# Kernel optimization log

Hardware: AMD Instinct MI355X
Metric: run time of the kernel (lower is better)

## Reference

```python
import jax, jax.numpy as jnp
import numpy as np

D_MODEL = 1024
N_HIDDEN = 64   # per-head dim (outer factor of packed proj dim)
N_HEAD = 16
B, L = 2, 2048


def setup_inputs() -> dict:
    key = jax.random.key(0)
    ks = jax.random.split(key, 7)
    s = 0.02
    return {
        "q": jax.random.normal(ks[0], (B, L, D_MODEL), dtype=jnp.float32),
        "k": jax.random.normal(ks[1], (B, L, D_MODEL), dtype=jnp.float32),
        "v": jax.random.normal(ks[2], (B, L, D_MODEL), dtype=jnp.float32),
        # torch nn.Linear weights: shape (out_features, in_features), y = x @ W.T
        "W_Q": jax.random.normal(ks[3], (N_HIDDEN * N_HEAD, D_MODEL), dtype=jnp.float32) * s,
        "W_K": jax.random.normal(ks[4], (N_HIDDEN * N_HEAD, D_MODEL), dtype=jnp.float32) * s,
        "W_V": jax.random.normal(ks[5], (N_HIDDEN * N_HEAD, D_MODEL), dtype=jnp.float32) * s,
        "W_O": jax.random.normal(ks[6], (D_MODEL, N_HEAD * N_HIDDEN), dtype=jnp.float32) * s,
    }


def reference(q, k, v, W_Q, W_K, W_V, W_O):
    b, l, _ = q.shape
    # projections (bias=False)
    qp = q @ W_Q.T  # [b,l,n_hidden*n_head]
    kp = k @ W_K.T
    vp = v @ W_V.T
    # rearrange 'b l (c h) -> b l c h' with c=n_hidden: hidden is OUTER factor
    qh = qp.reshape(b, l, N_HIDDEN, N_HEAD)
    kh = kp.reshape(b, l, N_HIDDEN, N_HEAD)
    vh = vp.reshape(b, l, N_HIDDEN, N_HEAD)
    scores = jnp.einsum('bldh,bjdh->bhlj', qh, kh) / np.float32(np.sqrt(N_HIDDEN))
    attn = jax.nn.softmax(scores, axis=-1)
    out = jnp.einsum('bhlj,bjdh->bldh', attn, vh)  # [b,l,n_hidden,n_head]
    out = out.reshape(b, l, N_HIDDEN * N_HEAD)      # 'b l d h -> b l (d h)'
    return out @ W_O.T
```

## Files before the change

### kernel.cpp

```cpp
#include <hip/hip_runtime.h>
#include <hip/hip_bf16.h>
#include <stdint.h>

typedef __attribute__((ext_vector_type(8))) short short8;
typedef __attribute__((ext_vector_type(4))) float f32x4;
typedef __attribute__((ext_vector_type(16))) float f32x16;
typedef __attribute__((ext_vector_type(2))) int int2v;
typedef unsigned short u16;
typedef unsigned int u32;


#define WAIT_VM12() do { asm volatile("s_waitcnt vmcnt(12)" ::: "memory"); \
                         __builtin_amdgcn_sched_barrier(0); } while (0)
#define WAIT_VM8()  do { asm volatile("s_waitcnt vmcnt(8)" ::: "memory"); \
                         __builtin_amdgcn_sched_barrier(0); } while (0)
#define WAIT_VM0()  do { asm volatile("s_waitcnt vmcnt(0)" ::: "memory"); \
                         __builtin_amdgcn_sched_barrier(0); } while (0)
#define BARRIER()   do { __builtin_amdgcn_s_barrier(); \
                         __builtin_amdgcn_sched_barrier(0); } while (0)
#define LGKM0_BAR() do { asm volatile("s_waitcnt lgkmcnt(0)" ::: "memory"); \
                         __builtin_amdgcn_s_barrier(); \
                         __builtin_amdgcn_sched_barrier(0); } while (0)

#define FSWZ(r) (((r) ^ ((r) >> 3)) & 7)

__device__ __forceinline__ u16 bf16rne(float f) {
  u32 u = __builtin_bit_cast(u32, f);
  u += 0x7FFFu + ((u >> 16) & 1u);
  return (u16)(u >> 16);
}

__device__ __forceinline__ u32 cvtpk(float lo, float hi) {
  u32 r;
  asm("v_cvt_pk_bf16_f32 %0, %1, %2" : "=v"(r) : "v"(lo), "v"(hi));
  return r;
}

__device__ __forceinline__ void gl_lds16(const u16* g, u16* l) {
  __builtin_amdgcn_global_load_lds((const __attribute__((address_space(1))) void*)g,
                                   (__attribute__((address_space(3))) void*)l, 16, 0, 0);
}

struct CastArgs {
  const float* src[4];
  u16* dst[4];
  int n4[4];
};

__global__ void cast_all(CastArgs a) {
  const int id = blockIdx.y;
  const float* __restrict__ s = a.src[id];
  u16* __restrict__ d = a.dst[id];
  const int stride = gridDim.x * blockDim.x;
  const int i0 = blockIdx.x * blockDim.x + threadIdx.x;
  if (id < 3) {
    const int n4 = a.n4[id];
    for (int i = i0; i < n4; i += stride) {
      float4 v = ((const float4*)s)[i];
      u32 lo = (u32)bf16rne(v.x) | ((u32)bf16rne(v.y) << 16);
      u32 hi = (u32)bf16rne(v.z) | ((u32)bf16rne(v.w) << 16);
      ((uint2*)d)[i] = make_uint2(lo, hi);
    }
  } else {
    const int n = a.n4[3];
    for (int i = i0; i < n; i += stride) {
      int row = i >> 10, c = i & 1023;
      int hh = c >> 6, dd = c & 63;
      d[i] = bf16rne(s[(row << 10) + dd * 16 + hh]);
    }
  }
}

struct ProjFArgs { const float* A[3]; const u16* W[3]; u16* D[3]; float scale[3]; };

__global__ __launch_bounds__(256, 2) void gemm_projf(ProjFArgs pa) {
  const int bid = blockIdx.x;
  const int grp = ((bid >> 6) << 3) | (bid & 7);
  const int bn = ((bid >> 3) & 7) * 128;
  const int z = grp >> 5;
  const int bm = (grp & 31) * 128;
  const float* __restrict__ A = pa.A[z];
  const u16* __restrict__ Bw = pa.W[z];
  u16* __restrict__ D = pa.D[z];
  const float ascale = pa.scale[z];
  const int epi = (z == 2) ? 1 : 0;

  const int tid = threadIdx.x, lane = tid & 63, w = tid >> 6;
  const int wr = w >> 1, wc = w & 1;
  __shared__ __align__(16) u16 As[2][128 * 64];
  __shared__ __align__(16) u16 Bs[2][128 * 64];

  f32x4 acc[4][4];
#pragma unroll
  for (int m = 0; m < 4; ++m)
#pragma unroll
    for (int n = 0; n < 4; ++n) acc[m][n] = (f32x4){0.f, 0.f, 0.f, 0.f};

  struct ARegs { float4 v[8]; };
  ARegs RA, RB;

  auto STAGE_A = [&](int kt, ARegs& R) {
#pragma unroll
    for (int i = 0; i < 4; ++i) {
      int c = tid + i * 256;
      int row = c >> 3;
      int col = (((c & 7) ^ (row & 7)) << 3);
      const float* src = A + (size_t)(bm + row) * 1024 + kt * 64 + col;
      R.v[2 * i] = *(const float4*)(src);
      R.v[2 * i + 1] = *(const float4*)(src + 4);
    }
  };
  auto WRITE_A = [&](ARegs& R, int b) {
#pragma unroll
    for (int i = 0; i < 4; ++i) {
      int c = tid + i * 256;
      u32 p0 = (u32)bf16rne(R.v[2 * i].x) | ((u32)bf16rne(R.v[2 * i].y) << 16);
      u32 p1 = (u32)bf16rne(R.v[2 * i].z) | ((u32)bf16rne(R.v[2 * i].w) << 16);
      u32 p2 = (u32)bf16rne(R.v[2 * i + 1].x) | ((u32)bf16rne(R.v[2 * i + 1].y) << 16);
      u32 p3 = (u32)bf16rne(R.v[2 * i + 1].z) | ((u32)bf16rne(R.v[2 * i + 1].w) << 16);
      *(uint4*)&As[b][c * 8] = make_uint4(p0, p1, p2, p3);
    }
  };
  auto STAGE_B = [&](int kt, int b) {
#pragma unroll
    for (int i = 0; i < 4; ++i) {
      int c = tid + i * 256;
      int row = c >> 3;
      int swz = (((c & 7) ^ (row & 7)) << 3);
      gl_lds16(Bw + (size_t)(bn + row) * 1024 + kt * 64 + swz, &Bs[b][c * 8]);
    }
  };
  auto COMPUTE = [&](int b) {
#pragma unroll
    for (int ks = 0; ks < 2; ++ks) {
      const int ck = ks * 4 + (lane >> 4);
      short8 af[4], bfr[4];
#pragma unroll
      for (int m = 0; m < 4; ++m) {
        int r = wr * 64 + m * 16 + (lane & 15);
        af[m] = *(const short8*)&As[b][(r * 8 + (ck ^ (r & 7))) * 8];
      }
#pragma unroll
      for (int n = 0; n < 4; ++n) {
        int r = wc * 64 + n * 16 + (lane & 15);
        bfr[n] = *(const short8*)&Bs[b][(r * 8 + (ck ^ (r & 7))) * 8];
      }
#pragma unroll
      for (int m = 0; m < 4; ++m)
#pragma unroll
        for (int n = 0; n < 4; ++n)
          acc[m][n] = __builtin_amdgcn_mfma_f32_16x16x32_bf16(af[m], bfr[n], acc[m][n], 0, 0, 0);
    }
  };

  STAGE_A(0, RA); STAGE_B(0, 0);
  STAGE_A(1, RB); STAGE_B(1, 1);
  for (int k2 = 0; k2 < 7; ++k2) {
    const int kt = 2 * k2;
    WAIT_VM12();
    WRITE_A(RA, 0); LGKM0_BAR();
    COMPUTE(0); BARRIER();
    STAGE_A(kt + 2, RA); STAGE_B(kt + 2, 0);
    WAIT_VM12();
    WRITE_A(RB, 1); LGKM0_BAR();
    COMPUTE(1); BARRIER();
    STAGE_A(kt + 3, RB); STAGE_B(kt + 3, 1);
  }
  WAIT_VM12();
  WRITE_A(RA, 0); LGKM0_BAR();
  COMPUTE(0); BARRIER();
  WAIT_VM0();
  WRITE_A(RB, 1); LGKM0_BAR();
  COMPUTE(1);

  const int lrow4 = (lane >> 4) << 2;
  const int h = lane & 15;
  if (epi == 0) {
    const int dbase = (bn + wc * 64) >> 4;
#pragma unroll
    for (int m = 0; m < 4; ++m)
#pragma unroll
      for (int i = 0; i < 4; ++i) {
        int R = bm + wr * 64 + m * 16 + lrow4 + i;
        int b = R >> 11, l = R & 2047;
        u32 lo = (u32)bf16rne(acc[m][0][i] * ascale) | ((u32)bf16rne(acc[m][1][i] * ascale) << 16);
        u32 hi = (u32)bf16rne(acc[m][2][i] * ascale) | ((u32)bf16rne(acc[m][3][i] * ascale) << 16);
        size_t addr = ((size_t)((b * 16 + h) * 2048 + l)) * 64 + dbase;
        *(uint2*)(D + addr) = make_uint2(lo, hi);
      }
  } else {
    const int dbase = (bn + wc * 64) >> 4;
    const int b = bm >> 11;
#pragma unroll
    for (int m = 0; m < 4; ++m) {
      int l0 = (bm & 2047) + wr * 64 + m * 16 + lrow4;
#pragma unroll
      for (int n = 0; n < 4; ++n) {
        int d = dbase + n;
        u32 lo = (u32)bf16rne(acc[m][n][0]) | ((u32)bf16rne(acc[m][n][1]) << 16);
        u32 hi = (u32)bf16rne(acc[m][n][2]) | ((u32)bf16rne(acc[m][n][3]) << 16);
        size_t addr = ((size_t)((b * 16 + h) * 64 + d)) * 2048 + l0;
        *(uint2*)(D + addr) = make_uint2(lo, hi);
      }
    }
  }
}

__global__ __launch_bounds__(256, 2) void gemm_oproj(const u16* __restrict__ A,
                                                     const u16* __restrict__ Bw,
                                                     float* __restrict__ C) {
  const int bid = blockIdx.x;
  const int slot = bid >> 3;
  const int bm = ((bid & 7) * 4 + (slot >> 3)) * 128;
  const int bn = (slot & 7) * 128;
  const int tid = threadIdx.x, lane = tid & 63, w = tid >> 6;
  const int wr = w >> 1, wc = w & 1;
  __shared__ __align__(16) u16 As[2][128 * 64];
  __shared__ __align__(16) u16 Bs[2][128 * 64];
  f32x4 acc[4][4];
#pragma unroll
  for (int m = 0; m < 4; ++m)
#pragma unroll
    for (int n = 0; n < 4; ++n) acc[m][n] = (f32x4){0.f, 0.f, 0.f, 0.f};

  auto STAGE = [&](int kt, int b) {
#pragma unroll
    for (int i = 0; i < 4; ++i) {
      int c = tid + i * 256;
      int row = c >> 3, kc = c & 7;
      int swz = (kc ^ (row & 7)) << 3;
      int bA = bm >> 11;
      int lrow = (bm & 2047) + row;
      const u16* srcA = A + ((size_t)(bA * 16 + kt) * 2048 + lrow) * 64 + swz;
      gl_lds16(srcA, &As[b][c * 8]);
      const u16* srcB = Bw + (size_t)(bn + row) * 1024 + kt * 64 + swz;
      gl_lds16(srcB, &Bs[b][c * 8]);
    }
  };

  auto COMPUTE = [&](int b) {
#pragma unroll
    for (int ks = 0; ks < 2; ++ks) {
      const int ck = ks * 4 + (lane >> 4);
      short8 af[4], bfr[4];
#pragma unroll
      for (int m = 0; m < 4; ++m) {
        int r = wr * 64 + m * 16 + (lane & 15);
        af[m] = *(const short8*)&As[b][(r * 8 + (ck ^ (r & 7))) * 8];
      }
#pragma unroll
      for (int n = 0; n < 4; ++n) {
        int r = wc * 64 + n * 16 + (lane & 15);
        bfr[n] = *(const short8*)&Bs[b][(r * 8 + (ck ^ (r & 7))) * 8];
      }
#pragma unroll
      for (int m = 0; m < 4; ++m)
#pragma unroll
        for (int n = 0; n < 4; ++n)
          acc[m][n] = __builtin_amdgcn_mfma_f32_16x16x32_bf16(af[m], bfr[n], acc[m][n], 0, 0, 0);
    }
  };

  STAGE(0, 0);
  STAGE(1, 1);
  for (int kt = 0; kt < 15; ++kt) {
    WAIT_VM8();
    BARRIER();
    COMPUTE(kt & 1);
    BARRIER();
    if (kt < 14) STAGE(kt + 2, kt & 1);
  }
  WAIT_VM0();
  BARRIER();
  COMPUTE(1);

  const int lrow4 = (lane >> 4) << 2;
#pragma unroll
  for (int m = 0; m < 4; ++m)
#pragma unroll
    for (int i = 0; i < 4; ++i) {
      int R = bm + wr * 64 + m * 16 + lrow4 + i;
      size_t base = (size_t)R * 1024 + bn + wc * 64 + (lane & 15);
#pragma unroll
      for (int n = 0; n < 4; ++n) C[base + n * 16] = acc[m][n][i];
    }
}

__global__ __launch_bounds__(128, 2) void attn_kernel(const u16* __restrict__ Qh,
                                                      const u16* __restrict__ Kh,
                                                      const u16* __restrict__ Vt,
                                                      u16* __restrict__ Oh) {
  const int hb = blockIdx.x;
  const int qt = blockIdx.y;
  const int tid = threadIdx.x, lane = tid & 63, w = tid >> 6;
  const int l31 = lane & 31, hi = lane >> 5;
  __shared__ __align__(16) u16 Ks[2][64 * 64];
  __shared__ __align__(16) u16 Vs[3][64 * 64];

  const u16* Qg = Qh + (size_t)hb * (2048 * 64);
  const u16* Kg = Kh + (size_t)hb * (2048 * 64);
  const u16* Vg = Vt + (size_t)hb * (64 * 2048);
  const int qrow = qt * 64 + w * 32 + l31;

  short8 qf[4];
#pragma unroll
  for (int ks = 0; ks < 4; ++ks)
    qf[ks] = *(const short8*)(Qg + (size_t)qrow * 64 + ks * 16 + hi * 8);

  int rs[4], sw[4];
#pragma unroll
  for (int i = 0; i < 4; ++i) {
    int c = tid + i * 128;
    rs[i] = c >> 3;
    sw[i] = (((c & 7) ^ FSWZ(rs[i])) << 3);
  }

  auto STAGE_K = [&](int t, int slot) {
    const size_t ko = (size_t)t * (64 * 64);
#pragma unroll
    for (int i = 0; i < 4; ++i) {
      int c = tid + i * 128;
      gl_lds16(Kg + ko + (size_t)rs[i] * 64 + sw[i], &Ks[slot][c * 8]);
    }
  };
  auto STAGE_V = [&](int t, int slot) {
    const int vo = t * 64;
#pragma unroll
    for (int i = 0; i < 4; ++i) {
      int c = tid + i * 128;
      gl_lds16(Vg + (size_t)rs[i] * 2048 + vo + sw[i], &Vs[slot][c * 8]);
    }
  };

  f32x16 oacc0, oacc1, SA0, SA1, SB0, SB1;
#pragma unroll
  for (int i = 0; i < 16; ++i) { oacc0[i] = 0.f; oacc1[i] = 0.f; }
  u32 pkA[16], pkB[16];
  float lrow = 0.f;

  auto QKT = [&](int kslot, f32x16& s0, f32x16& s1) {
#pragma unroll
    for (int i = 0; i < 16; ++i) { s0[i] = 0.f; s1[i] = 0.f; }
    __builtin_amdgcn_s_setprio(1);
#pragma unroll
    for (int ks = 0; ks < 4; ++ks) {
      const int ck = 2 * ks + hi;
      const int r0 = l31, r1 = 32 + l31;
      short8 k0 = *(const short8*)&Ks[kslot][(r0 * 8 + (ck ^ FSWZ(r0))) * 8];
      short8 k1 = *(const short8*)&Ks[kslot][(r1 * 8 + (ck ^ FSWZ(r1))) * 8];
      s0 = __builtin_amdgcn_mfma_f32_32x32x16_bf16(k0, qf[ks], s0, 0, 0, 0);
      s1 = __builtin_amdgcn_mfma_f32_32x32x16_bf16(k1, qf[ks], s1, 0, 0, 0);
    }
    __builtin_amdgcn_s_setprio(0);
  };

  auto PV = [&](const u32* pk, int vslot) {
    __builtin_amdgcn_s_setprio(1);
#pragma unroll
    for (int c = 0; c < 4; ++c) {
      union { u32 wu[4]; short8 v; } un;
      un.wu[0] = pk[c * 4 + 0]; un.wu[1] = pk[c * 4 + 1];
      un.wu[2] = pk[c * 4 + 2]; un.wu[3] = pk[c * 4 + 3];
      const int ckv = 2 * c + hi;
      const int rv0 = l31, rv1 = 32 + l31;
      short8 v0 = *(const short8*)&Vs[vslot][(rv0 * 8 + (ckv ^ FSWZ(rv0))) * 8];
      short8 v1 = *(const short8*)&Vs[vslot][(rv1 * 8 + (ckv ^ FSWZ(rv1))) * 8];
      oacc0 = __builtin_amdgcn_mfma_f32_32x32x16_bf16(v0, un.v, oacc0, 0, 0, 0);
      oacc1 = __builtin_amdgcn_mfma_f32_32x32x16_bf16(v1, un.v, oacc1, 0, 0, 0);
    }
    __builtin_amdgcn_s_setprio(0);
  };

  auto SOFTMAX = [&](f32x16& s0, f32x16& s1, u32* pk) {
#pragma unroll
    for (int i = 0; i < 16; ++i) {
      s0[i] = __builtin_amdgcn_exp2f(s0[i]);
      s1[i] = __builtin_amdgcn_exp2f(s1[i]);
    }
    f32x16 a01 = s0 + s1;
    float r8[8];
#pragma unroll
    for (int i = 0; i < 8; ++i) r8[i] = a01[i] + a01[i + 8];
#pragma unroll
    for (int i = 0; i < 4; ++i) r8[i] += r8[i + 4];
    float rsum = (r8[0] + r8[1]) + (r8[2] + r8[3]);
    int2v pr = __builtin_amdgcn_permlane32_swap(__builtin_bit_cast(int, rsum),
                                                __builtin_bit_cast(int, rsum), false, false);
    lrow += __builtin_bit_cast(float, pr[0]) + __builtin_bit_cast(float, pr[1]);
#pragma unroll
    for (int c = 0; c < 4; ++c) {
      float pe0, pe1, pe2, pe3, pe4, pe5, pe6, pe7;
      if (c < 2) {
        const int s8 = (c & 1) * 8;
        pe0 = s0[s8 + 0]; pe1 = s0[s8 + 1]; pe2 = s0[s8 + 2]; pe3 = s0[s8 + 3];
        pe4 = s0[s8 + 4]; pe5 = s0[s8 + 5]; pe6 = s0[s8 + 6]; pe7 = s0[s8 + 7];
      } else {
        const int s8 = (c & 1) * 8;
        pe0 = s1[s8 + 0]; pe1 = s1[s8 + 1]; pe2 = s1[s8 + 2]; pe3 = s1[s8 + 3];
        pe4 = s1[s8 + 4]; pe5 = s1[s8 + 5]; pe6 = s1[s8 + 6]; pe7 = s1[s8 + 7];
      }
      u32 a0 = cvtpk(pe0, pe1), a1 = cvtpk(pe2, pe3);
      u32 a2 = cvtpk(pe4, pe5), a3 = cvtpk(pe6, pe7);
      int2v w02 = __builtin_amdgcn_permlane32_swap((int)a0, (int)a2, false, false);
      int2v w13 = __builtin_amdgcn_permlane32_swap((int)a1, (int)a3, false, false);
      pk[c * 4 + 0] = (u32)w02[0]; pk[c * 4 + 1] = (u32)w13[0];
      pk[c * 4 + 2] = (u32)w02[1]; pk[c * 4 + 3] = (u32)w13[1];
    }
  };

  STAGE_K(0, 0); STAGE_K(1, 1); STAGE_V(0, 0);
  WAIT_VM8(); BARRIER();
  QKT(0, SA0, SA1);
  BARRIER();
  STAGE_K(2, 0); STAGE_V(1, 1);
  WAIT_VM8(); BARRIER();
  QKT(1, SB0, SB1);
  SOFTMAX(SA0, SA1, pkB);
  BARRIER();
  STAGE_K(3, 1); STAGE_V(2, 2);

  for (int i = 2; i < 32; i += 2) {
    WAIT_VM8(); BARRIER();
    QKT(0, SA0, SA1);
    PV(pkB, (i - 2) % 3);
    SOFTMAX(SB0, SB1, pkA);
    BARRIER();
    if (i + 2 <= 31) STAGE_K(i + 2, 0);
    STAGE_V(i + 1, (i + 1) % 3);
    WAIT_VM8(); BARRIER();
    QKT(1, SB0, SB1);
    PV(pkA, (i - 1) % 3);
    SOFTMAX(SA0, SA1, pkB);
    BARRIER();
    if (i + 3 <= 31) STAGE_K(i + 3, 1);
    if (i + 2 <= 31) STAGE_V(i + 2, (i + 2) % 3);
  }

  WAIT_VM0(); BARRIER();
  SOFTMAX(SB0, SB1, pkA);
  PV(pkB, 30 % 3);
  PV(pkA, 31 % 3);

  const float inv = 1.0f / lrow;
  u16* Og = Oh + (size_t)hb * (2048 * 64) + (size_t)qrow * 64;
#pragma unroll
  for (int dblk = 0; dblk < 2; ++dblk) {
#pragma unroll
    for (int r = 0; r < 16; r += 2) {
      const int d = dblk * 32 + (r & 3) + 8 * (r >> 2) + 4 * hi;
      float v0 = (dblk ? oacc1[r] : oacc0[r]) * inv;
      float v1 = (dblk ? oacc1[r + 1] : oacc0[r + 1]) * inv;
      *(u32*)(Og + d) = (u32)bf16rne(v0) | ((u32)bf16rne(v1) << 16);
    }
  }
}

extern "C" void kernel_launch(void* const* d_in, const int* in_sizes, int n_in,
                              void* d_out, int out_size, void* d_ws, size_t ws_size,
                              hipStream_t stream) {
  const float* q = (const float*)d_in[0];
  const float* k = (const float*)d_in[1];
  const float* v = (const float*)d_in[2];
  const float* WQ = (const float*)d_in[3];
  const float* WK = (const float*)d_in[4];
  const float* WV = (const float*)d_in[5];
  const float* WO = (const float*)d_in[6];
  float* out = (float*)d_out;
  char* ws = (char*)d_ws;
  const size_t MB = 1024 * 1024;
  if (ws_size < 64 * MB) return;

  u16* WQb = (u16*)(ws + 24 * MB);
  u16* WKb = (u16*)(ws + 26 * MB);
  u16* WVb = (u16*)(ws + 28 * MB);
  u16* WOt = (u16*)(ws + 30 * MB);
  u16* Qh  = (u16*)(ws + 32 * MB);
  u16* Kh  = (u16*)(ws + 40 * MB);
  u16* Vt  = (u16*)(ws + 48 * MB);
  u16* Ohd = (u16*)(ws + 56 * MB);

  CastArgs ca;
  ca.src[0] = WQ; ca.dst[0] = WQb; ca.n4[0] = (1024 * 1024) / 4;
  ca.src[1] = WK; ca.dst[1] = WKb; ca.n4[1] = (1024 * 1024) / 4;
  ca.src[2] = WV; ca.dst[2] = WVb; ca.n4[2] = (1024 * 1024) / 4;
  ca.src[3] = WO; ca.dst[3] = WOt; ca.n4[3] = 1024 * 1024;
  cast_all<<<dim3(128, 4), 256, 0, stream>>>(ca);

  ProjFArgs pa;
  pa.A[0] = q; pa.W[0] = WQb; pa.D[0] = Qh;  pa.scale[0] = 0.18033688011f;
  pa.A[1] = k; pa.W[1] = WKb; pa.D[1] = Kh;  pa.scale[1] = 1.0f;
  pa.A[2] = v; pa.W[2] = WVb; pa.D[2] = Vt;  pa.scale[2] = 1.0f;
  gemm_projf<<<768, 256, 0, stream>>>(pa);

  attn_kernel<<<dim3(32, 32), 128, 0, stream>>>(Qh, Kh, Vt, Ohd);

  gemm_oproj<<<256, 256, 0, stream>>>(Ohd, WOt, out);
}
```

Baseline: 128.5 us.

## Reorder GEMM main loop to overlap LDS writes and loads with MFMA compute

Restructures the double-buffered projection GEMM loop so each iteration waits once, issues the next B stage and A prefetch, writes the other A buffer to LDS, and then computes on the current buffer. This drops the separate barrier after each compute and lets LDS writes and global loads proceed alongside the MFMA work. In exchange it waits for all outstanding loads (vmcnt(0)) each half-iteration instead of vmcnt(12), which can expose global load latency, and the buffer hazards now depend on a single barrier per step.

```diff
diff --git a/kernel.cpp b/kernel.cpp
--- a/kernel.cpp
+++ b/kernel.cpp
@@ -153,24 +153,33 @@
     }
   };
 
-  STAGE_A(0, RA); STAGE_B(0, 0);
-  STAGE_A(1, RB); STAGE_B(1, 1);
+  STAGE_A(0, RA);
+  STAGE_B(0, 0);
+  STAGE_A(1, RB);
+  WAIT_VM12();
+  WRITE_A(RA, 0);
+
   for (int k2 = 0; k2 < 7; ++k2) {
-    const int kt = 2 * k2;
-    WAIT_VM12();
-    WRITE_A(RA, 0); LGKM0_BAR();
-    COMPUTE(0); BARRIER();
-    STAGE_A(kt + 2, RA); STAGE_B(kt + 2, 0);
-    WAIT_VM12();
-    WRITE_A(RB, 1); LGKM0_BAR();
-    COMPUTE(1); BARRIER();
-    STAGE_A(kt + 3, RB); STAGE_B(kt + 3, 1);
-  }
-  WAIT_VM12();
-  WRITE_A(RA, 0); LGKM0_BAR();
-  COMPUTE(0); BARRIER();
+    WAIT_VM0();
+    LGKM0_BAR();
+    STAGE_B(2 * k2 + 1, 1);
+    STAGE_A(2 * k2 + 2, RA);
+    WRITE_A(RB, 1);
+    COMPUTE(0);
+    WAIT_VM0();
+    LGKM0_BAR();
+    STAGE_B(2 * k2 + 2, 0);
+    STAGE_A(2 * k2 + 3, RB);
+    WRITE_A(RA, 0);
+    COMPUTE(1);
+  }
   WAIT_VM0();
-  WRITE_A(RB, 1); LGKM0_BAR();
+  LGKM0_BAR();
+  STAGE_B(15, 1);
+  WRITE_A(RB, 1);
+  COMPUTE(0);
+  WAIT_VM0();
+  LGKM0_BAR();
   COMPUTE(1);
 
   const int lrow4 = (lane >> 4) << 2;
```

Result: slower. 132.3 us (+3.0%).
